# Optimization experiments

Hardware: AMD Instinct MI355X
Metric: run time of the kernel (lower is better)

The kernel has to match this reference:

```python
import jax, jax.numpy as jnp
import numpy as np
import math

EPS = 1.1920929e-07  # torch F.rms_norm default eps = fp32 machine epsilon


def rms_norm(x):
    # normalize over last dim, no learned weight (matches F.rms_norm(x, (d,)))
    var = jnp.mean(jnp.square(x), axis=-1, keepdims=True)
    return x * jax.lax.rsqrt(var + EPS)


def rotary(x, cos, sin):
    # x: (B, T, H, D); cos/sin: (T, D) -> broadcast over B, H
    d2 = x.shape[-1] // 2
    x1, x2 = x[..., :d2], x[..., d2:]
    rot = jnp.concatenate([-x2, x1], axis=-1)  # rotate_half
    c = cos[None, :, None, :]
    s = sin[None, :, None, :]
    return x * c + rot * s


def setup_inputs() -> dict:
    key = jax.random.key(0)
    ks = jax.random.split(key, 5)
    B, T, C, H = 2, 2048, 1024, 16
    D = C // H
    x = jax.random.normal(ks[0], (B, T, C), dtype=jnp.float32)
    # real RoPE tables (theta=10000), duplicated across the two halves
    inv_freq = 1.0 / (10000.0 ** (np.arange(0, D, 2, dtype=np.float32) / D))
    pos = np.arange(T, dtype=np.float32)
    freqs = np.outer(pos, inv_freq)            # (T, D/2)
    emb = np.concatenate([freqs, freqs], -1)   # (T, D)
    cos = jnp.asarray(np.cos(emb), dtype=jnp.float32)
    sin = jnp.asarray(np.sin(emb), dtype=jnp.float32)
    sc_in = 1.0 / math.sqrt(C)
    W_attn = jax.random.normal(ks[1], (C, 3 * C), dtype=jnp.float32) * sc_in
    b_attn = jax.random.normal(ks[2], (3 * C,), dtype=jnp.float32) * 0.02
    W_proj = jax.random.normal(ks[3], (C, C), dtype=jnp.float32) * sc_in
    b_proj = jax.random.normal(ks[4], (C,), dtype=jnp.float32) * 0.02
    return {"x": x, "cos": cos, "sin": sin, "W_attn": W_attn, "b_attn": b_attn,
            "W_proj": W_proj, "b_proj": b_proj}


def reference(x, cos, sin, W_attn, b_attn, W_proj, b_proj):
    B, T, C = x.shape
    H = 16
    D = C // H
    qkv = x @ W_attn + b_attn                         # (B, T, 3C)
    qkv = qkv.reshape(B, T, 3, H, D)                  # 'b t (a h d) -> ...'
    q, k, v = qkv[:, :, 0], qkv[:, :, 1], qkv[:, :, 2]  # (B, T, H, D)
    q, k = rms_norm(q), rms_norm(k)
    q = rotary(q, cos, sin)
    k = rotary(k, cos, sin)
    # causal SDPA, scale = 1/sqrt(D)
    scale = 1.0 / math.sqrt(D)
    scores = jnp.einsum('bthd,bshd->bhts', q, k) * scale  # (B, H, T, T)
    causal = jnp.tril(jnp.ones((T, T), dtype=bool))
    scores = jnp.where(causal[None, None], scores, jnp.finfo(scores.dtype).min)
    attn = jax.nn.softmax(scores, axis=-1)
    y = jnp.einsum('bhts,bshd->bthd', attn, v)            # (B, T, H, D)
    y = y.reshape(B, T, C)
    return y @ W_proj + b_proj
```

## Files before the change

### kernel.cpp

```cpp
#include <hip/hip_runtime.h>
#include <math.h>

#define EPSV 1.1920929e-07f

typedef __attribute__((ext_vector_type(8))) short short8;
typedef __attribute__((ext_vector_type(4))) float f32x4;

__device__ __forceinline__ float bf2f(unsigned short u) {
    union { unsigned int i; float f; } c; c.i = ((unsigned int)u) << 16; return c.f;
}
__device__ __forceinline__ unsigned short f2bf(float f) {
    union { float f; unsigned int i; } c; c.f = f;
    unsigned int r = c.i + 0x7FFFu + ((c.i >> 16) & 1u);
    return (unsigned short)(r >> 16);
}
__device__ __forceinline__ unsigned int pack_bf16_ru(float a, float b) {
    union { float f; unsigned int i; } ca, cb; ca.f = a; cb.f = b;
    return __builtin_amdgcn_perm(cb.i + 0x8000u, ca.i + 0x8000u, 0x07060302u);
}
__device__ __forceinline__ void async_lds16(const unsigned short* g, unsigned short* l) {
    __builtin_amdgcn_global_load_lds(
        (const __attribute__((address_space(1))) unsigned int*)g,
        (__attribute__((address_space(3))) unsigned int*)l, 16, 0, 0);
}

__global__ __launch_bounds__(256) void cast_bf16(
    const float* __restrict__ src, unsigned short* __restrict__ dst, int n)
{
    const int i = (blockIdx.x * 256 + threadIdx.x) * 4;
    if (i >= n) return;
    const float4 v = *(const float4*)&src[i];
    ushort4 o;
    o.x = f2bf(v.x); o.y = f2bf(v.y); o.z = f2bf(v.z); o.w = f2bf(v.w);
    *(ushort4*)&dst[i] = o;
}

__global__ __launch_bounds__(256) void transpose_cast(
    const float* __restrict__ W, unsigned short* __restrict__ Wt, int K, int N)
{
    __shared__ float tile[32][33];
    const int n0 = blockIdx.x * 32, k0 = blockIdx.y * 32;
    const int r = threadIdx.x >> 3, c4 = (threadIdx.x & 7) * 4;
    const float4 v = *(const float4*)&W[(size_t)(k0 + r) * N + n0 + c4];
    tile[r][c4 + 0] = v.x; tile[r][c4 + 1] = v.y;
    tile[r][c4 + 2] = v.z; tile[r][c4 + 3] = v.w;
    __syncthreads();
    ushort4 o;
    o.x = f2bf(tile[c4 + 0][r]); o.y = f2bf(tile[c4 + 1][r]);
    o.z = f2bf(tile[c4 + 2][r]); o.w = f2bf(tile[c4 + 3][r]);
    *(ushort4*)&Wt[(size_t)(n0 + r) * K + k0 + c4] = o;
}

template <bool OUT_BF16>
__global__ __launch_bounds__(256) void gemm_bf16(
    const unsigned short* __restrict__ A,
    const unsigned short* __restrict__ Bt,
    const float* __restrict__ bias,
    void* __restrict__ Cv,
    int M, int N, int K)
{
    __shared__ unsigned short As[128][32];
    __shared__ unsigned short Bs[128][32];
    const int t    = threadIdx.x;
    const int lane = t & 63;
    const int wv   = t >> 6;
    const int wrow = (wv >> 1) * 64;
    const int wcol = (wv & 1) * 64;
    const int m0 = blockIdx.y * 128;
    const int n0 = blockIdx.x * 128;
    const int col  = lane & 15;
    const int quad = lane >> 4;

    const int srow = (wv << 5) + (lane >> 2);
    const int scol = (lane & 3) << 3;
    const unsigned short* ap0 = A  + (size_t)(m0 + srow) * K + scol;
    const unsigned short* ap1 = ap0 + (size_t)16 * K;
    const unsigned short* bp0 = Bt + (size_t)(n0 + srow) * K + scol;
    const unsigned short* bp1 = bp0 + (size_t)16 * K;
    unsigned short* al0 = &As[srow][scol];
    unsigned short* al1 = &As[srow + 16][scol];
    unsigned short* bl0 = &Bs[srow][scol];
    unsigned short* bl1 = &Bs[srow + 16][scol];

    f32x4 acc[4][4];
    #pragma unroll
    for (int i = 0; i < 4; ++i)
        #pragma unroll
        for (int j = 0; j < 4; ++j)
            acc[i][j] = (f32x4){0.f, 0.f, 0.f, 0.f};

    for (int k0 = 0; k0 < K; k0 += 32) {
        async_lds16(ap0, al0);
        async_lds16(ap1, al1);
        async_lds16(bp0, bl0);
        async_lds16(bp1, bl1);
        ap0 += 32; ap1 += 32; bp0 += 32; bp1 += 32;
        __syncthreads();
        short8 af[4], bf[4];
        #pragma unroll
        for (int mt = 0; mt < 4; ++mt)
            af[mt] = *(const short8*)&As[wrow + mt * 16 + col][quad << 3];
        #pragma unroll
        for (int nt = 0; nt < 4; ++nt)
            bf[nt] = *(const short8*)&Bs[wcol + nt * 16 + col][quad << 3];
        #pragma unroll
        for (int mt = 0; mt < 4; ++mt)
            #pragma unroll
            for (int nt = 0; nt < 4; ++nt)
                acc[mt][nt] = __builtin_amdgcn_mfma_f32_16x16x32_bf16(
                    af[mt], bf[nt], acc[mt][nt], 0, 0, 0);
        __syncthreads();
    }

    const int rowq = quad << 2;
    #pragma unroll
    for (int nt = 0; nt < 4; ++nt) {
        const int n = n0 + wcol + nt * 16 + col;
        const float bv = bias[n];
        #pragma unroll
        for (int mt = 0; mt < 4; ++mt) {
            #pragma unroll
            for (int r = 0; r < 4; ++r) {
                const int m = m0 + wrow + mt * 16 + rowq + r;
                const float v = acc[mt][nt][r] + bv;
                if (OUT_BF16)
                    ((unsigned short*)Cv)[(size_t)m * N + n] = f2bf(v);
                else
                    ((float*)Cv)[(size_t)m * N + n] = v;
            }
        }
    }
}

__global__ __launch_bounds__(256) void gemm_bf16_n64(
    const unsigned short* __restrict__ A,
    const unsigned short* __restrict__ Bt,
    const float* __restrict__ bias,
    float* __restrict__ C,
    int M, int N, int K)
{
    __shared__ unsigned short As[128][32];
    __shared__ unsigned short Bs[64][32];
    const int t    = threadIdx.x;
    const int lane = t & 63;
    const int wv   = t >> 6;
    const int wrow = wv << 5;
    const int m0 = blockIdx.y * 128;
    const int n0 = blockIdx.x * 64;
    const int col  = lane & 15;
    const int quad = lane >> 4;

    const int srow = (wv << 5) + (lane >> 2);
    const int scol = (lane & 3) << 3;
    const unsigned short* ap0 = A  + (size_t)(m0 + srow) * K + scol;
    const unsigned short* ap1 = ap0 + (size_t)16 * K;
    const int bsrow = (wv << 4) + (lane >> 2);
    const unsigned short* bp0 = Bt + (size_t)(n0 + bsrow) * K + scol;
    unsigned short* al0 = &As[srow][scol];
    unsigned short* al1 = &As[srow + 16][scol];
    unsigned short* bl0 = &Bs[bsrow][scol];

    f32x4 acc[2][4];
    #pragma unroll
    for (int i = 0; i < 2; ++i)
        #pragma unroll
        for (int j = 0; j < 4; ++j)
            acc[i][j] = (f32x4){0.f, 0.f, 0.f, 0.f};

    for (int k0 = 0; k0 < K; k0 += 32) {
        async_lds16(ap0, al0);
        async_lds16(ap1, al1);
        async_lds16(bp0, bl0);
        ap0 += 32; ap1 += 32; bp0 += 32;
        __syncthreads();
        short8 af[2], bf[4];
        #pragma unroll
        for (int mt = 0; mt < 2; ++mt)
            af[mt] = *(const short8*)&As[wrow + mt * 16 + col][quad << 3];
        #pragma unroll
        for (int nt = 0; nt < 4; ++nt)
            bf[nt] = *(const short8*)&Bs[nt * 16 + col][quad << 3];
        #pragma unroll
        for (int mt = 0; mt < 2; ++mt)
            #pragma unroll
            for (int nt = 0; nt < 4; ++nt)
                acc[mt][nt] = __builtin_amdgcn_mfma_f32_16x16x32_bf16(
                    af[mt], bf[nt], acc[mt][nt], 0, 0, 0);
        __syncthreads();
    }

    const int rowq = quad << 2;
    #pragma unroll
    for (int nt = 0; nt < 4; ++nt) {
        const int n = n0 + nt * 16 + col;
        const float bv = bias[n];
        #pragma unroll
        for (int mt = 0; mt < 2; ++mt) {
            #pragma unroll
            for (int r = 0; r < 4; ++r) {
                const int m = m0 + wrow + mt * 16 + rowq + r;
                C[(size_t)m * N + n] = acc[mt][nt][r] + bv;
            }
        }
    }
}

__global__ __launch_bounds__(256) void rmsnorm_rope(
    unsigned short* __restrict__ qkv, const float* __restrict__ cosp,
    const float* __restrict__ sinp, int BT, int T)
{
    const int wid  = (blockIdx.x << 2) + (threadIdx.x >> 6);
    const int lane = threadIdx.x & 63;
    const int hq = wid & 3;
    const int w  = (wid >> 2) & 1;
    const int bt = wid >> 3;
    if (bt >= BT) return;
    const int h  = (hq << 2) + (lane >> 4);
    const int d4 = (lane & 15) << 2;
    const int tpos = bt % T;
    const size_t idx = (size_t)bt * 3072 + (w << 10) + (h << 6) + d4;

    const ushort4 u = *(const ushort4*)&qkv[idx];
    const float x0 = bf2f(u.x), x1 = bf2f(u.y), x2 = bf2f(u.z), x3 = bf2f(u.w);
    float ss = x0 * x0 + x1 * x1 + x2 * x2 + x3 * x3;
    ss += __shfl_xor(ss, 1, 64);
    ss += __shfl_xor(ss, 2, 64);
    ss += __shfl_xor(ss, 4, 64);
    ss += __shfl_xor(ss, 8, 64);
    const float rn = rsqrtf(ss * (1.0f / 64.0f) + EPSV);
    const float xn0 = x0 * rn, xn1 = x1 * rn, xn2 = x2 * rn, xn3 = x3 * rn;
    const float p0 = __shfl_xor(xn0, 8, 64);
    const float p1 = __shfl_xor(xn1, 8, 64);
    const float p2 = __shfl_xor(xn2, 8, 64);
    const float p3 = __shfl_xor(xn3, 8, 64);
    const float sgn = (d4 < 32) ? -1.0f : 1.0f;
    const float4 c = *(const float4*)&cosp[tpos * 64 + d4];
    const float4 s = *(const float4*)&sinp[tpos * 64 + d4];
    const float scale = (w == 0) ? 0.18033688011112042f : 1.0f;
    ushort4 o;
    o.x = f2bf(fmaf(xn0, c.x, sgn * p0 * s.x) * scale);
    o.y = f2bf(fmaf(xn1, c.y, sgn * p1 * s.y) * scale);
    o.z = f2bf(fmaf(xn2, c.z, sgn * p2 * s.z) * scale);
    o.w = f2bf(fmaf(xn3, c.w, sgn * p3 * s.w) * scale);
    *(ushort4*)&qkv[idx] = o;
}

__global__ __launch_bounds__(256) void v_transpose(
    const unsigned short* __restrict__ qkv, unsigned short* __restrict__ vt,
    int T)
{
    __shared__ unsigned short tile[64][72];
    const int bh = blockIdx.x;
    const int b  = bh >> 4, h = bh & 15;
    const int t0 = blockIdx.y << 6;
    const int t  = threadIdx.x;
    const unsigned short* vbase = qkv + (size_t)b * T * 3072 + 2048 + (h << 6);

    #pragma unroll
    for (int i = 0; i < 2; ++i) {
        const int c = t + (i << 8);
        const int r = c >> 3, c8 = (c & 7) << 3;
        const short8 v = *(const short8*)&vbase[(size_t)(t0 + r) * 3072 + c8];
        #pragma unroll
        for (int j = 0; j < 8; ++j)
            tile[c8 + j][r] = (unsigned short)v[j];
    }
    __syncthreads();
    #pragma unroll
    for (int i = 0; i < 2; ++i) {
        const int c = t + (i << 8);
        const int d = c >> 3, c8 = (c & 7) << 3;
        const short8 o = *(const short8*)&tile[d][c8];
        *(short8*)&vt[((size_t)bh * 64 + d) * T + t0 + c8] = o;
    }
}

__global__ __launch_bounds__(256) void flash_attn_mfma(
    const unsigned short* __restrict__ qkv,
    const unsigned short* __restrict__ vt,
    unsigned short* __restrict__ yb,
    int B, int T)
{
    const int bh = blockIdx.x;
    const int b  = bh >> 4, h = bh & 15;
    const int q0 = ((int)gridDim.y - 1 - (int)blockIdx.y) << 6;
    const int t  = threadIdx.x;
    const int lane = t & 63;
    const int w    = t >> 6;
    const int col  = lane & 15;
    const int quad = lane >> 4;

    __shared__ unsigned short Ks [64][72];
    __shared__ unsigned short Vts[64][72];
    __shared__ unsigned short Ps [4][16][72];

    const unsigned short* qb  = qkv + (size_t)b * T * 3072 + (h << 6);
    const unsigned short* kb  = qb + 1024;
    const unsigned short* vtb = vt + (size_t)bh * 64 * T;

    const int qw = q0 + w * 16;
    const int qg = qw + col;

    short8 qf[2];
    {
        const unsigned short* qrow = qb + (size_t)qg * 3072 + (quad << 3);
        qf[0] = *(const short8*)&qrow[0];
        qf[1] = *(const short8*)&qrow[32];
    }

    f32x4 oacc[4];
    #pragma unroll
    for (int i = 0; i < 4; ++i) oacc[i] = (f32x4){0.f, 0.f, 0.f, 0.f};
    float m_i = -INFINITY, l_i = 0.f;

    const int sr = t >> 3, sc = (t & 7) << 3;
    const unsigned short* kp0 = kb  + (size_t)sr * 3072 + sc;
    const unsigned short* kp1 = kp0 + (size_t)32 * 3072;
    const unsigned short* vp0 = vtb + (size_t)sr * T + sc;
    const unsigned short* vp1 = vp0 + (size_t)32 * T;
    unsigned short* kw0 = &Ks[sr][sc];
    unsigned short* kw1 = &Ks[sr + 32][sc];
    unsigned short* vw0 = &Vts[sr][sc];
    unsigned short* vw1 = &Vts[sr + 32][sc];
    unsigned short* pw  = &Ps[w][col][0];

    const int last_kt = q0 >> 6;
    for (int kt = 0; kt <= last_kt; ++kt) {
        const int k0 = kt << 6;
        __syncthreads();
        *(short8*)kw0 = *(const short8*)kp0;
        *(short8*)kw1 = *(const short8*)kp1;
        *(short8*)vw0 = *(const short8*)vp0;
        *(short8*)vw1 = *(const short8*)vp1;
        kp0 += 64 * 3072; kp1 += 64 * 3072; vp0 += 64; vp1 += 64;
        __syncthreads();

        f32x4 st[4];
        #pragma unroll
        for (int i = 0; i < 4; ++i) st[i] = (f32x4){0.f, 0.f, 0.f, 0.f};
        #pragma unroll
        for (int ks = 0; ks < 2; ++ks)
            #pragma unroll
            for (int mt = 0; mt < 4; ++mt) {
                const short8 kf = *(const short8*)&Ks[mt * 16 + col][ks * 32 + (quad << 3)];
                st[mt] = __builtin_amdgcn_mfma_f32_16x16x32_bf16(kf, qf[ks], st[mt], 0, 0, 0);
            }

        float sv[4][4];
        float mloc = -INFINITY;
        if (k0 + 63 > qw) {
            #pragma unroll
            for (int mt = 0; mt < 4; ++mt) {
                const int sbase = k0 + mt * 16 + (quad << 2);
                #pragma unroll
                for (int r = 0; r < 4; ++r) {
                    float x = st[mt][r];
                    if (sbase + r > qg) x = -INFINITY;
                    sv[mt][r] = x;
                    mloc = fmaxf(mloc, x);
                }
            }
        } else {
            #pragma unroll
            for (int mt = 0; mt < 4; ++mt)
                #pragma unroll
                for (int r = 0; r < 4; ++r) {
                    sv[mt][r] = st[mt][r];
                    mloc = fmaxf(mloc, st[mt][r]);
                }
        }
        mloc = fmaxf(mloc, __shfl_xor(mloc, 16, 64));
        mloc = fmaxf(mloc, __shfl_xor(mloc, 32, 64));
        const float mnew  = fmaxf(m_i, mloc);
        const float alpha = __builtin_amdgcn_exp2f(m_i - mnew);
        float rs = 0.f;
        #pragma unroll
        for (int mt = 0; mt < 4; ++mt) {
            const float p0 = __builtin_amdgcn_exp2f(sv[mt][0] - mnew);
            const float p1 = __builtin_amdgcn_exp2f(sv[mt][1] - mnew);
            const float p2 = __builtin_amdgcn_exp2f(sv[mt][2] - mnew);
            const float p3 = __builtin_amdgcn_exp2f(sv[mt][3] - mnew);
            rs += (p0 + p1) + (p2 + p3);
            uint2 pk;
            pk.x = pack_bf16_ru(p0, p1);
            pk.y = pack_bf16_ru(p2, p3);
            *(uint2*)&pw[mt * 16 + (quad << 2)] = pk;
        }
        rs += __shfl_xor(rs, 16, 64);
        rs += __shfl_xor(rs, 32, 64);
        l_i = l_i * alpha + rs;
        m_i = mnew;
        #pragma unroll
        for (int mt = 0; mt < 4; ++mt) {
            oacc[mt][0] *= alpha; oacc[mt][1] *= alpha;
            oacc[mt][2] *= alpha; oacc[mt][3] *= alpha;
        }

        #pragma unroll
        for (int ks = 0; ks < 2; ++ks) {
            const short8 pf = *(const short8*)&pw[ks * 32 + (quad << 3)];
            #pragma unroll
            for (int mt = 0; mt < 4; ++mt) {
                const short8 vf = *(const short8*)&Vts[mt * 16 + col][ks * 32 + (quad << 3)];
                oacc[mt] = __builtin_amdgcn_mfma_f32_16x16x32_bf16(vf, pf, oacc[mt], 0, 0, 0);
            }
        }
    }

    const float inv = 1.0f / l_i;
    unsigned short* yrow = yb + (size_t)(b * T + qg) * 1024 + (h << 6);
    #pragma unroll
    for (int mt = 0; mt < 4; ++mt) {
        ushort4 yv;
        yv.x = f2bf(oacc[mt][0] * inv);
        yv.y = f2bf(oacc[mt][1] * inv);
        yv.z = f2bf(oacc[mt][2] * inv);
        yv.w = f2bf(oacc[mt][3] * inv);
        *(ushort4*)&yrow[mt * 16 + (quad << 2)] = yv;
    }
}

extern "C" void kernel_launch(void* const* d_in, const int* in_sizes, int n_in,
                              void* d_out, int out_size, void* d_ws, size_t ws_size,
                              hipStream_t stream)
{
    const float* x      = (const float*)d_in[0];
    const float* cosp   = (const float*)d_in[1];
    const float* sinp   = (const float*)d_in[2];
    const float* W_attn = (const float*)d_in[3];
    const float* b_attn = (const float*)d_in[4];
    const float* W_proj = (const float*)d_in[5];
    const float* b_proj = (const float*)d_in[6];
    float* out = (float*)d_out;

    const int C = 1024, H = 16;
    const int T  = in_sizes[1] / 64;
    const int BT = in_sizes[0] / C;
    const int B  = BT / T;

    unsigned short* qkvb = (unsigned short*)d_ws;
    unsigned short* xb   = qkvb + (size_t)BT * 3072;
    unsigned short* Wab  = xb   + (size_t)BT * 1024;
    unsigned short* Wpb  = Wab  + (size_t)3072 * 1024;
    unsigned short* yb   = Wpb  + (size_t)1024 * 1024;
    unsigned short* vtb  = xb;

    cast_bf16<<<dim3(BT * C / 1024), dim3(256), 0, stream>>>(x, xb, BT * C);
    transpose_cast<<<dim3(3 * C / 32, C / 32), dim3(256), 0, stream>>>(W_attn, Wab, C, 3 * C);
    transpose_cast<<<dim3(C / 32, C / 32), dim3(256), 0, stream>>>(W_proj, Wpb, C, C);

    gemm_bf16<true><<<dim3(3 * C / 128, BT / 128), dim3(256), 0, stream>>>(
        xb, Wab, b_attn, qkvb, BT, 3 * C, C);

    rmsnorm_rope<<<dim3(BT * 2), dim3(256), 0, stream>>>(
        qkvb, cosp, sinp, BT, T);

    v_transpose<<<dim3(B * H, T / 64), dim3(256), 0, stream>>>(qkvb, vtb, T);

    flash_attn_mfma<<<dim3(B * H, T / 64), dim3(256), 0, stream>>>(
        qkvb, vtb, yb, B, T);

    gemm_bf16_n64<<<dim3(C / 64, BT / 128), dim3(256), 0, stream>>>(
        yb, Wpb, b_proj, out, BT, C, C);
}
```

Before: 207.3 us.

## Drop online-softmax max tracking, prefetch K/V into registers, merge weight transposes

```diff
diff --git a/kernel.cpp b/kernel.cpp
--- a/kernel.cpp
+++ b/kernel.cpp
@@ -35,11 +35,16 @@
     *(ushort4*)&dst[i] = o;
 }
 
-__global__ __launch_bounds__(256) void transpose_cast(
-    const float* __restrict__ W, unsigned short* __restrict__ Wt, int K, int N)
+__global__ __launch_bounds__(256) void transpose_cast_both(
+    const float* __restrict__ Wa, unsigned short* __restrict__ Wat,
+    const float* __restrict__ Wp, unsigned short* __restrict__ Wpt)
 {
     __shared__ float tile[32][33];
-    const int n0 = blockIdx.x * 32, k0 = blockIdx.y * 32;
+    int bx = blockIdx.x;
+    const float* W; unsigned short* Wt; int N;
+    if (bx < 96) { W = Wa; Wt = Wat; N = 3072; }
+    else         { W = Wp; Wt = Wpt; N = 1024; bx -= 96; }
+    const int n0 = bx * 32, k0 = blockIdx.y * 32;
     const int r = threadIdx.x >> 3, c4 = (threadIdx.x & 7) * 4;
     const float4 v = *(const float4*)&W[(size_t)(k0 + r) * N + n0 + c4];
     tile[r][c4 + 0] = v.x; tile[r][c4 + 1] = v.y;
@@ -48,7 +53,7 @@
     ushort4 o;
     o.x = f2bf(tile[c4 + 0][r]); o.y = f2bf(tile[c4 + 1][r]);
     o.z = f2bf(tile[c4 + 2][r]); o.w = f2bf(tile[c4 + 3][r]);
-    *(ushort4*)&Wt[(size_t)(n0 + r) * K + k0 + c4] = o;
+    *(ushort4*)&Wt[(size_t)(n0 + r) * 1024 + k0 + c4] = o;
 }
 
 template <bool OUT_BF16>
@@ -311,7 +316,7 @@
     f32x4 oacc[4];
     #pragma unroll
     for (int i = 0; i < 4; ++i) oacc[i] = (f32x4){0.f, 0.f, 0.f, 0.f};
-    float m_i = -INFINITY, l_i = 0.f;
+    float l_i = 0.f;
 
     const int sr = t >> 3, sc = (t & 7) << 3;
     const unsigned short* kp0 = kb  + (size_t)sr * 3072 + sc;
@@ -324,16 +329,27 @@
     unsigned short* vw1 = &Vts[sr + 32][sc];
     unsigned short* pw  = &Ps[w][col][0];
 
+    short8 rk0 = *(const short8*)kp0;
+    short8 rk1 = *(const short8*)kp1;
+    short8 rv0 = *(const short8*)vp0;
+    short8 rv1 = *(const short8*)vp1;
+
     const int last_kt = q0 >> 6;
     for (int kt = 0; kt <= last_kt; ++kt) {
         const int k0 = kt << 6;
         __syncthreads();
-        *(short8*)kw0 = *(const short8*)kp0;
-        *(short8*)kw1 = *(const short8*)kp1;
-        *(short8*)vw0 = *(const short8*)vp0;
-        *(short8*)vw1 = *(const short8*)vp1;
-        kp0 += 64 * 3072; kp1 += 64 * 3072; vp0 += 64; vp1 += 64;
-        __syncthreads();
+        *(short8*)kw0 = rk0;
+        *(short8*)kw1 = rk1;
+        *(short8*)vw0 = rv0;
+        *(short8*)vw1 = rv1;
+        __syncthreads();
+        if (kt < last_kt) {
+            kp0 += 64 * 3072; kp1 += 64 * 3072; vp0 += 64; vp1 += 64;
+            rk0 = *(const short8*)kp0;
+            rk1 = *(const short8*)kp1;
+            rv0 = *(const short8*)vp0;
+            rv1 = *(const short8*)vp1;
+        }
 
         f32x4 st[4];
         #pragma unroll
@@ -346,40 +362,22 @@
                 st[mt] = __builtin_amdgcn_mfma_f32_16x16x32_bf16(kf, qf[ks], st[mt], 0, 0, 0);
             }
 
-        float sv[4][4];
-        float mloc = -INFINITY;
-        if (k0 + 63 > qw) {
-            #pragma unroll
-            for (int mt = 0; mt < 4; ++mt) {
+        const bool diag = (k0 + 63 > qw);
+        float rs = 0.f;
+        #pragma unroll
+        for (int mt = 0; mt < 4; ++mt) {
+            float x0 = st[mt][0], x1 = st[mt][1], x2 = st[mt][2], x3 = st[mt][3];
+            if (diag) {
                 const int sbase = k0 + mt * 16 + (quad << 2);
-                #pragma unroll
-                for (int r = 0; r < 4; ++r) {
-                    float x = st[mt][r];
-                    if (sbase + r > qg) x = -INFINITY;
-                    sv[mt][r] = x;
-                    mloc = fmaxf(mloc, x);
-                }
+                if (sbase + 0 > qg) x0 = -INFINITY;
+                if (sbase + 1 > qg) x1 = -INFINITY;
+                if (sbase + 2 > qg) x2 = -INFINITY;
+                if (sbase + 3 > qg) x3 = -INFINITY;
             }
-        } else {
-            #pragma unroll
-            for (int mt = 0; mt < 4; ++mt)
-                #pragma unroll
-                for (int r = 0; r < 4; ++r) {
-                    sv[mt][r] = st[mt][r];
-                    mloc = fmaxf(mloc, st[mt][r]);
-                }
-        }
-        mloc = fmaxf(mloc, __shfl_xor(mloc, 16, 64));
-        mloc = fmaxf(mloc, __shfl_xor(mloc, 32, 64));
-        const float mnew  = fmaxf(m_i, mloc);
-        const float alpha = __builtin_amdgcn_exp2f(m_i - mnew);
-        float rs = 0.f;
-        #pragma unroll
-        for (int mt = 0; mt < 4; ++mt) {
-            const float p0 = __builtin_amdgcn_exp2f(sv[mt][0] - mnew);
-            const float p1 = __builtin_amdgcn_exp2f(sv[mt][1] - mnew);
-            const float p2 = __builtin_amdgcn_exp2f(sv[mt][2] - mnew);
-            const float p3 = __builtin_amdgcn_exp2f(sv[mt][3] - mnew);
+            const float p0 = __builtin_amdgcn_exp2f(x0);
+            const float p1 = __builtin_amdgcn_exp2f(x1);
+            const float p2 = __builtin_amdgcn_exp2f(x2);
+            const float p3 = __builtin_amdgcn_exp2f(x3);
             rs += (p0 + p1) + (p2 + p3);
             uint2 pk;
             pk.x = pack_bf16_ru(p0, p1);
@@ -388,13 +386,7 @@
         }
         rs += __shfl_xor(rs, 16, 64);
         rs += __shfl_xor(rs, 32, 64);
-        l_i = l_i * alpha + rs;
-        m_i = mnew;
-        #pragma unroll
-        for (int mt = 0; mt < 4; ++mt) {
-            oacc[mt][0] *= alpha; oacc[mt][1] *= alpha;
-            oacc[mt][2] *= alpha; oacc[mt][3] *= alpha;
-        }
+        l_i += rs;
 
         #pragma unroll
         for (int ks = 0; ks < 2; ++ks) {
@@ -446,8 +438,8 @@
     unsigned short* vtb  = xb;
 
     cast_bf16<<<dim3(BT * C / 1024), dim3(256), 0, stream>>>(x, xb, BT * C);
-    transpose_cast<<<dim3(3 * C / 32, C / 32), dim3(256), 0, stream>>>(W_attn, Wab, C, 3 * C);
-    transpose_cast<<<dim3(C / 32, C / 32), dim3(256), 0, stream>>>(W_proj, Wpb, C, C);
+    transpose_cast_both<<<dim3(128, 32), dim3(256), 0, stream>>>(
+        W_attn, Wab, W_proj, Wpb);
 
     gemm_bf16<true><<<dim3(3 * C / 128, BT / 128), dim3(256), 0, stream>>>(
         xb, Wab, b_attn, qkvb, BT, 3 * C, C);
```

Measured after the change: 202.5 us. -2.3%, faster.
